# Optimization experiments

Measured on AMD Instinct MI355X. Metric: run time of the kernel, lower is better.

The kernel has to match this reference:

```python
import jax, jax.numpy as jnp
import numpy as np

B, N, D, H = 4, 8192, 1024, 16
C = D // H  # head dim = 64
EPS = 1e-6


def setup_inputs() -> dict:
    key = jax.random.key(0)
    ks = jax.random.split(key, 8)
    sc = 0.02
    return {
        "q": jax.random.normal(ks[0], (B, N, D), jnp.float32),
        "k": jax.random.normal(ks[1], (B, N, D), jnp.float32),
        "v": jax.random.normal(ks[2], (B, N, D), jnp.float32),
        "Wq": jax.random.normal(ks[3], (D, D), jnp.float32) * sc,
        "Wk": jax.random.normal(ks[4], (D, D), jnp.float32) * sc,
        "Wv": jax.random.normal(ks[5], (D, D), jnp.float32) * sc,
        "Wproj": jax.random.normal(ks[6], (D, D), jnp.float32) * sc,
        "focusing_factor": jnp.asarray(3.0, jnp.float32),
    }


def _to_heads(x):
    # b n (h c) -> (b h) n c
    return x.reshape(B, N, H, C).transpose(0, 2, 1, 3).reshape(B * H, N, C)


def reference(q, k, v, Wq, Wk, Wv, Wproj, focusing_factor):
    # projections (torch Linear: x @ W.T, no bias)
    qp = q @ Wq.T
    kp = k @ Wk.T
    vp = v @ Wv.T

    def feature_map(x):
        # |GELU(x)| + eps, then focused renormalization:
        # softmax(focusing_factor * log(f)) * mean(f)
        f = jnp.abs(jax.nn.gelu(x, approximate=False)) + EPS
        f_norm = f.mean(axis=-1, keepdims=True)
        return jax.nn.softmax(jnp.log(f) * focusing_factor, axis=-1) * f_norm

    qf = feature_map(qp)
    kf = feature_map(kp)

    qh = _to_heads(qf)  # [B*H, N, C]
    kh = _to_heads(kf)
    vh = _to_heads(vp)

    k_mean = kh.mean(axis=1)  # [B*H, C]
    z_inv = jnp.einsum('bnd,bd->bn', qh, k_mean) + EPS  # [B*H, N]

    # (k/sqrt(N))^T (v/sqrt(N)) == (k^T v)/N
    kv = jnp.einsum('bnc,bnd->bcd', kh, vh) / N  # [B*H, C, C]
    y = jnp.einsum('bic,bcd->bid', qh, kv) / z_inv[..., None]  # [B*H, N, C]

    y = y.reshape(B, H, N, C).transpose(0, 2, 1, 3).reshape(B, N, D)
    return y @ Wproj.T
```

## Files before the change

kernel.cpp:

```cpp
#include <hip/hip_runtime.h>

using f16 = _Float16;
typedef __attribute__((ext_vector_type(4))) _Float16 f16x4;
typedef __attribute__((ext_vector_type(8))) _Float16 f16x8;
typedef __attribute__((ext_vector_type(4))) float f32x4;

#define DEVI __device__ __forceinline__

namespace {

constexpr int BB = 4;
constexpr int NN = 8192;
constexpr int DD = 1024;
constexpr int MTOT = BB * NN;
constexpr float FSCALE = 64.0f;
constexpr float ZCONST = 64.0f * 64.0f * (8192.0f * 1e-6f);

DEVI void gl16(const void* g, void* l) {
  __builtin_amdgcn_global_load_lds(
      (__attribute__((address_space(1))) void*)(void*)g,
      (__attribute__((address_space(3))) void*)l, 16, 0, 0);
}

DEVI float wsum(float v) {
#pragma unroll
  for (int m = 32; m > 0; m >>= 1) v += __shfl_xor(v, m, 64);
  return v;
}
DEVI float wmaxr(float v) {
#pragma unroll
  for (int m = 32; m > 0; m >>= 1) v = fmaxf(v, __shfl_xor(v, m, 64));
  return v;
}
DEVI float block_sum(float v, float* sred, int tid) {
  v = wsum(v);
  __syncthreads();
  if ((tid & 63) == 0) sred[tid >> 6] = v;
  __syncthreads();
  return sred[0] + sred[1] + sred[2] + sred[3];
}
DEVI float block_max(float v, float* sred, int tid) {
  v = wmaxr(v);
  __syncthreads();
  if ((tid & 63) == 0) sred[tid >> 6] = v;
  __syncthreads();
  return fmaxf(fmaxf(sred[0], sred[1]), fmaxf(sred[2], sred[3]));
}

struct CastArgs {
  const float* src[8];
  f16* dst[8];
  int n4[8];
};

__global__ __launch_bounds__(256) void cast_kernel(CastArgs a) {
  const int z = blockIdx.y;
  const float4* __restrict__ s = (const float4*)a.src[z];
  f16x4* __restrict__ d = (f16x4*)a.dst[z];
  const int n4 = a.n4[z];
  for (int i = blockIdx.x * blockDim.x + threadIdx.x; i < n4;
       i += gridDim.x * blockDim.x) {
    float4 f = s[i];
    f16x4 o = {(f16)f.x, (f16)f.y, (f16)f.z, (f16)f.w};
    d[i] = o;
  }
}

struct Gemm3 {
  const f16* A[3];
  const f16* Bt[3];
  void* C[3];
};

template <typename OutT>
__global__ __launch_bounds__(512, 2) void gemm256(Gemm3 P) {
  constexpr int K = DD;
  constexpr int N = DD;
  constexpr int NKT = K / 64;
  const int z = blockIdx.z;
  const f16* __restrict__ A = P.A[z];
  const f16* __restrict__ Bt = P.Bt[z];
  OutT* __restrict__ C = (OutT*)P.C[z];

  const int nx = gridDim.x;
  int lin = blockIdx.y * nx + blockIdx.x;
  const int cpx = (gridDim.y * nx) >> 3;
  lin = (lin & 7) * cpx + (lin >> 3);
  const size_t row0 = (size_t)(lin / nx) * 256;
  const size_t col0 = (size_t)(lin % nx) * 256;

  const int tid = threadIdx.x, lane = tid & 63, wv = tid >> 6;
  const int wm = wv >> 2, wn = wv & 3;
  const int fr = lane & 15, f7 = lane & 7, kq = lane >> 4;

  __shared__ __align__(16) f16 LA[2][2][8192];
  __shared__ __align__(16) f16 LB[2][2][8192];

  const int srow = wv * 8 + (lane >> 3);
  const int ssw = (lane & 7) ^ ((lane >> 3) & 7);

  auto stageA = [&](int kts, int half) {
    const f16* src = A + (row0 + half * 128 + srow) * K + kts * 64 + ssw * 8;
    f16* dst = &LA[kts & 1][half][wv * 512];
#pragma unroll
    for (int c = 0; c < 2; ++c) gl16(src + (size_t)c * 64 * K, dst + c * 4096);
  };
  auto stageB = [&](int kts, int half) {
    const f16* src = Bt + (col0 + half * 128 + srow) * K + kts * 64 + ssw * 8;
    f16* dst = &LB[kts & 1][half][wv * 512];
#pragma unroll
    for (int c = 0; c < 2; ++c) gl16(src + (size_t)c * 64 * K, dst + c * 4096);
  };

  f32x4 acc[8][4];
#pragma unroll
  for (int i = 0; i < 8; ++i)
#pragma unroll
    for (int j = 0; j < 4; ++j) acc[i][j] = f32x4{0.f, 0.f, 0.f, 0.f};

  stageA(0, 0); stageA(0, 1); stageB(0, 0); stageB(0, 1);
  stageA(1, 0); stageA(1, 1);
  asm volatile("s_waitcnt vmcnt(4)" ::: "memory");
  __builtin_amdgcn_s_barrier();

  const int c0e = (kq ^ f7) * 8;
#pragma unroll 2
  for (int kt = 0; kt < NKT; ++kt) {
    const int buf = kt & 1;
    const f16* Ah = LA[buf][wm];
    const f16* Bh = &LB[buf][wn >> 1][(wn & 1) * 4096];
    f16x8 a0[8], a1[8], b0[4], b1[4];

#pragma unroll
    for (int mi = 0; mi < 8; ++mi)
      a0[mi] = *(const f16x8*)&Ah[(mi * 16 + fr) * 64 + c0e];
#pragma unroll
    for (int ni = 0; ni < 4; ++ni)
      b0[ni] = *(const f16x8*)&Bh[(ni * 16 + fr) * 64 + c0e];
    if (kt < NKT - 1) stageB(kt + 1, 0);
    __builtin_amdgcn_s_barrier();
    asm volatile("s_waitcnt lgkmcnt(0)" ::: "memory");
    __builtin_amdgcn_s_setprio(1);
#pragma unroll
    for (int mi = 0; mi < 4; ++mi)
#pragma unroll
      for (int ni = 0; ni < 4; ++ni)
        acc[mi][ni] = __builtin_amdgcn_mfma_f32_16x16x32_f16(
            a0[mi], b0[ni], acc[mi][ni], 0, 0, 0);
    __builtin_amdgcn_s_setprio(0);
    __builtin_amdgcn_s_barrier();

#pragma unroll
    for (int mi = 0; mi < 8; ++mi)
      a1[mi] = *(const f16x8*)&Ah[(mi * 16 + fr) * 64 + (c0e ^ 32)];
    if (kt < NKT - 1) stageB(kt + 1, 1);
    __builtin_amdgcn_s_barrier();
    asm volatile("s_waitcnt lgkmcnt(0)" ::: "memory");
    __builtin_amdgcn_s_setprio(1);
#pragma unroll
    for (int mi = 4; mi < 8; ++mi)
#pragma unroll
      for (int ni = 0; ni < 4; ++ni)
        acc[mi][ni] = __builtin_amdgcn_mfma_f32_16x16x32_f16(
            a0[mi], b0[ni], acc[mi][ni], 0, 0, 0);
    __builtin_amdgcn_s_setprio(0);
    __builtin_amdgcn_s_barrier();

#pragma unroll
    for (int ni = 0; ni < 4; ++ni)
      b1[ni] = *(const f16x8*)&Bh[(ni * 16 + fr) * 64 + (c0e ^ 32)];
    if (kt < NKT - 2) stageA(kt + 2, 0);
    __builtin_amdgcn_s_barrier();
    asm volatile("s_waitcnt lgkmcnt(0)" ::: "memory");
    __builtin_amdgcn_s_setprio(1);
#pragma unroll
    for (int mi = 0; mi < 4; ++mi)
#pragma unroll
      for (int ni = 0; ni < 4; ++ni)
        acc[mi][ni] = __builtin_amdgcn_mfma_f32_16x16x32_f16(
            a1[mi], b1[ni], acc[mi][ni], 0, 0, 0);
    __builtin_amdgcn_s_setprio(0);
    __builtin_amdgcn_s_barrier();

    if (kt < NKT - 2) stageA(kt + 2, 1);
    __builtin_amdgcn_s_barrier();
    __builtin_amdgcn_s_setprio(1);
#pragma unroll
    for (int mi = 4; mi < 8; ++mi)
#pragma unroll
      for (int ni = 0; ni < 4; ++ni)
        acc[mi][ni] = __builtin_amdgcn_mfma_f32_16x16x32_f16(
            a1[mi], b1[ni], acc[mi][ni], 0, 0, 0);
    __builtin_amdgcn_s_setprio(0);
    if (kt < NKT - 2)
      asm volatile("s_waitcnt vmcnt(4)" ::: "memory");
    else
      asm volatile("s_waitcnt vmcnt(0)" ::: "memory");
    __builtin_amdgcn_s_barrier();
  }

#pragma unroll
  for (int mi = 0; mi < 8; ++mi)
#pragma unroll
    for (int ni = 0; ni < 4; ++ni) {
      const size_t colv = col0 + wn * 64 + ni * 16 + fr;
#pragma unroll
      for (int r = 0; r < 4; ++r) {
        const size_t rowv = row0 + wm * 128 + mi * 16 + (lane >> 4) * 4 + r;
        C[rowv * N + colv] = (OutT)acc[mi][ni][r];
      }
    }
}

__global__ __launch_bounds__(256) void feature_kernel(
    const f16* __restrict__ qp, const f16* __restrict__ kp,
    f16* __restrict__ qf, f16* __restrict__ kf, const float* __restrict__ ffp) {
  const int row = blockIdx.x;
  const int tid = threadIdx.x;
  const bool isq = (blockIdx.y == 0);
  const f16* __restrict__ src = isq ? qp : kp;
  f16* __restrict__ dst = isq ? qf : kf;
  const float ff = ffp[0];
  __shared__ float sred[4];

  f16x4 xv = ((const f16x4*)src)[(size_t)row * 256 + tid];
  float f0[4];
  float ps = 0.f;
#pragma unroll
  for (int j = 0; j < 4; ++j) {
    float x = (float)xv[j];
    float g = 0.5f * x * (1.0f + erff(x * 0.70710678118654752f));
    float fv = fabsf(g) + 1e-6f;
    f0[j] = fv;
    ps += fv;
  }
  float fsum = block_sum(ps, sred, tid);
  float t[4];
  float pm = -1e30f;
#pragma unroll
  for (int j = 0; j < 4; ++j) {
    t[j] = ff * __logf(f0[j]);
    pm = fmaxf(pm, t[j]);
  }
  float tmax = block_max(pm, sred, tid);
  float e[4];
  float es = 0.f;
#pragma unroll
  for (int j = 0; j < 4; ++j) {
    e[j] = __expf(t[j] - tmax);
    es += e[j];
  }
  float esum = block_sum(es, sred, tid);
  const float scale = fsum * (1.0f / 1024.0f) / esum * FSCALE;
  f16x4 o;
#pragma unroll
  for (int j = 0; j < 4; ++j) o[j] = (f16)(e[j] * scale);
  ((f16x4*)dst)[(size_t)row * 256 + tid] = o;
}

__global__ __launch_bounds__(256) void kv_kernel(
    const f16* __restrict__ kf, const f16* __restrict__ vp,
    float* __restrict__ kvsum, float* __restrict__ colsum) {
  const int bh = blockIdx.x;
  const int b = bh >> 4, h = bh & 15;
  const int tid = threadIdx.x, lane = tid & 63, wave = tid >> 6;
  __shared__ __align__(16) f16 kt[32 * 64];
  __shared__ __align__(16) f16 vt[32 * 64];
  __shared__ float csred[4][64];

  f32x4 acc[4];
#pragma unroll
  for (int ni = 0; ni < 4; ++ni) acc[ni] = f32x4{0.f, 0.f, 0.f, 0.f};
  float cpart = 0.f;

  const int srow = wave * 8 + (lane >> 3);
  const int scol = (lane & 7) * 8;
  const int colbase = h * 64;
  const int n0base = blockIdx.y * 512;

  for (int n0 = n0base; n0 < n0base + 512; n0 += 32) {
    const size_t gofs = ((size_t)(b * NN + n0 + srow)) * DD + colbase + scol;
    gl16(kf + gofs, &kt[wave * 512]);
    gl16(vp + gofs, &vt[wave * 512]);
    __syncthreads();
    {
      const int c = tid & 63;
      const int r0 = (tid >> 6) * 8;
#pragma unroll
      for (int rr = 0; rr < 8; ++rr) cpart += (float)kt[(r0 + rr) * 64 + c];
    }
    f16x8 a, bfr[4];
#pragma unroll
    for (int j = 0; j < 8; ++j)
      a[j] = kt[((lane >> 4) * 8 + j) * 64 + wave * 16 + (lane & 15)];
#pragma unroll
    for (int ni = 0; ni < 4; ++ni)
#pragma unroll
      for (int j = 0; j < 8; ++j)
        bfr[ni][j] = vt[((lane >> 4) * 8 + j) * 64 + ni * 16 + (lane & 15)];
#pragma unroll
    for (int ni = 0; ni < 4; ++ni)
      acc[ni] = __builtin_amdgcn_mfma_f32_16x16x32_f16(a, bfr[ni], acc[ni], 0, 0, 0);
    __syncthreads();
  }
#pragma unroll
  for (int ni = 0; ni < 4; ++ni)
#pragma unroll
    for (int r = 0; r < 4; ++r) {
      const int c = wave * 16 + (lane >> 4) * 4 + r;
      const int d = ni * 16 + (lane & 15);
      atomicAdd(&kvsum[(size_t)bh * 4096 + c * 64 + d], acc[ni][r]);
    }
  csred[tid >> 6][tid & 63] = cpart;
  __syncthreads();
  if (tid < 64)
    atomicAdd(&colsum[bh * 64 + tid],
              csred[0][tid] + csred[1][tid] + csred[2][tid] + csred[3][tid]);
}

__global__ __launch_bounds__(256) void y_kernel(
    const f16* __restrict__ qf, const f16* __restrict__ kv16,
    const float* __restrict__ colsum, f16* __restrict__ y) {
  const int bh = blockIdx.x, b = bh >> 4, h = bh & 15;
  const int n0 = blockIdx.y * 128;
  const int tid = threadIdx.x, lane = tid & 63, wave = tid >> 6;
  __shared__ __align__(16) f16 qs[128 * 64];
  __shared__ __align__(16) f16 kvs[64 * 64];
  __shared__ float cs[64];
  __shared__ float zr[128];

#pragma unroll
  for (int cc = 0; cc < 4; ++cc) {
    const int r = wave * 32 + cc * 8 + (lane >> 3);
    gl16(qf + ((size_t)(b * NN + n0 + r)) * DD + h * 64 + (lane & 7) * 8,
         &qs[(wave * 4 + cc) * 512]);
  }
#pragma unroll
  for (int cc = 0; cc < 2; ++cc) {
    const int r = wave * 16 + cc * 8 + (lane >> 3);
    gl16(kv16 + (size_t)bh * 4096 + r * 64 + (lane & 7) * 8,
         &kvs[(wave * 2 + cc) * 512]);
  }
  if (tid < 64) cs[tid] = colsum[bh * 64 + tid];
  __syncthreads();
  if (tid < 128) {
    float zv = 0.f;
    for (int cc = 0; cc < 64; ++cc) {
      const int c = (cc + tid) & 63;
      zv += (float)qs[tid * 64 + c] * cs[c];
    }
    zr[tid] = zv + ZCONST;
  }
  __syncthreads();

  f32x4 acc[2][4];
#pragma unroll
  for (int mi = 0; mi < 2; ++mi)
#pragma unroll
    for (int ni = 0; ni < 4; ++ni) acc[mi][ni] = f32x4{0.f, 0.f, 0.f, 0.f};

#pragma unroll
  for (int ks = 0; ks < 2; ++ks) {
    f16x8 a[2], bfr[4];
#pragma unroll
    for (int mi = 0; mi < 2; ++mi)
      a[mi] = *(const f16x8*)&qs[(wave * 32 + mi * 16 + (lane & 15)) * 64 +
                                 ks * 32 + (lane >> 4) * 8];
#pragma unroll
    for (int ni = 0; ni < 4; ++ni)
#pragma unroll
      for (int j = 0; j < 8; ++j)
        bfr[ni][j] = kvs[(ks * 32 + (lane >> 4) * 8 + j) * 64 + ni * 16 + (lane & 15)];
#pragma unroll
    for (int mi = 0; mi < 2; ++mi)
#pragma unroll
      for (int ni = 0; ni < 4; ++ni)
        acc[mi][ni] = __builtin_amdgcn_mfma_f32_16x16x32_f16(
            a[mi], bfr[ni], acc[mi][ni], 0, 0, 0);
  }
#pragma unroll
  for (int mi = 0; mi < 2; ++mi)
#pragma unroll
    for (int ni = 0; ni < 4; ++ni)
#pragma unroll
      for (int r = 0; r < 4; ++r) {
        const int rrow = wave * 32 + mi * 16 + (lane >> 4) * 4 + r;
        const int d = ni * 16 + (lane & 15);
        const float yv = acc[mi][ni][r] / zr[rrow];
        y[((size_t)(b * NN + n0 + rrow)) * DD + h * 64 + d] = (f16)yv;
      }
}

}

extern "C" void kernel_launch(void* const* d_in, const int* in_sizes, int n_in,
                              void* d_out, int out_size, void* d_ws, size_t ws_size,
                              hipStream_t stream) {
  const float* q = (const float*)d_in[0];
  const float* k = (const float*)d_in[1];
  const float* v = (const float*)d_in[2];
  const float* Wq = (const float*)d_in[3];
  const float* Wk = (const float*)d_in[4];
  const float* Wv = (const float*)d_in[5];
  const float* Wp = (const float*)d_in[6];
  const float* ffp = (const float*)d_in[7];

  char* w = (char*)d_ws;
  size_t off = 0;
  auto alloc = [&](size_t b) {
    void* p = (void*)(w + off);
    off += (b + 255) & ~(size_t)255;
    return p;
  };
  const size_t big = (size_t)MTOT * DD * sizeof(f16);
  f16* q16 = (f16*)alloc(big);
  f16* k16 = (f16*)alloc(big);
  f16* v16 = (f16*)alloc(big);
  f16* qp16 = (f16*)alloc(big);
  f16* kp16 = (f16*)alloc(big);
  f16* vp16 = (f16*)alloc(big);
  f16* Wq16 = (f16*)alloc((size_t)DD * DD * 2);
  f16* Wk16 = (f16*)alloc((size_t)DD * DD * 2);
  f16* Wv16 = (f16*)alloc((size_t)DD * DD * 2);
  f16* Wp16 = (f16*)alloc((size_t)DD * DD * 2);
  float* kvsum = (float*)alloc(64 * 64 * 64 * sizeof(float));
  float* colsum = (float*)alloc(64 * 64 * sizeof(float));
  f16* kv16 = (f16*)alloc(64 * 64 * 64 * sizeof(f16));
  if (off > ws_size) return;

  f16* qf = q16;
  f16* kf = k16;
  f16* y16 = v16;

  CastArgs ca{};
  ca.src[0] = q;  ca.dst[0] = q16;  ca.n4[0] = MTOT * DD / 4;
  ca.src[1] = k;  ca.dst[1] = k16;  ca.n4[1] = MTOT * DD / 4;
  ca.src[2] = v;  ca.dst[2] = v16;  ca.n4[2] = MTOT * DD / 4;
  ca.src[3] = Wq; ca.dst[3] = Wq16; ca.n4[3] = DD * DD / 4;
  ca.src[4] = Wk; ca.dst[4] = Wk16; ca.n4[4] = DD * DD / 4;
  ca.src[5] = Wv; ca.dst[5] = Wv16; ca.n4[5] = DD * DD / 4;
  ca.src[6] = Wp; ca.dst[6] = Wp16; ca.n4[6] = DD * DD / 4;
  cast_kernel<<<dim3(1024, 7), 256, 0, stream>>>(ca);

  Gemm3 gp{};
  gp.A[0] = q16; gp.Bt[0] = Wq16; gp.C[0] = qp16;
  gp.A[1] = k16; gp.Bt[1] = Wk16; gp.C[1] = kp16;
  gp.A[2] = v16; gp.Bt[2] = Wv16; gp.C[2] = vp16;
  gemm256<f16><<<dim3(DD / 256, MTOT / 256, 3), 512, 0, stream>>>(gp);

  feature_kernel<<<dim3(MTOT, 2), 256, 0, stream>>>(qp16, kp16, qf, kf, ffp);

  hipMemsetAsync(kvsum, 0, 64 * 64 * 64 * sizeof(float) + 64 * 64 * sizeof(float),
                 stream);
  kv_kernel<<<dim3(64, 16), 256, 0, stream>>>(kf, vp16, kvsum, colsum);

  CastArgs cb{};
  cb.src[0] = kvsum; cb.dst[0] = kv16; cb.n4[0] = 64 * 64 * 64 / 4;
  cast_kernel<<<dim3(64, 1), 256, 0, stream>>>(cb);

  y_kernel<<<dim3(64, 64), 256, 0, stream>>>(qf, kv16, colsum, y16);

  Gemm3 gf{};
  gf.A[0] = y16; gf.Bt[0] = Wp16; gf.C[0] = d_out;
  gemm256<float><<<dim3(DD / 256, MTOT / 256, 1), 512, 0, stream>>>(gf);
}
```

Baseline: 700.3 us.

## Restructure GEMM main loop to single-barrier one-ahead prefetch

The GEMM inner loop now issues the whole next k-tile (A and B halves) into the alternate LDS buffer at the start of each iteration. It then loads all A/B fragments for both k-halves up front and runs the MFMAs in two batches gated by partial lgkmcnt waits, with a single barrier per iteration. This replaces the previous schedule, which used four interleaved barriers and prefetched A two tiles ahead. The aim is to cut barrier and synchronisation overhead and let the MFMAs issue in longer runs. The cost is a shallower prefetch distance for A and higher register pressure from holding all fragments at once.

```diff
diff --git a/kernel.cpp b/kernel.cpp
--- a/kernel.cpp
+++ b/kernel.cpp
@@ -119,83 +119,59 @@
     for (int j = 0; j < 4; ++j) acc[i][j] = f32x4{0.f, 0.f, 0.f, 0.f};
 
   stageA(0, 0); stageA(0, 1); stageB(0, 0); stageB(0, 1);
-  stageA(1, 0); stageA(1, 1);
-  asm volatile("s_waitcnt vmcnt(4)" ::: "memory");
+  asm volatile("s_waitcnt vmcnt(0)" ::: "memory");
   __builtin_amdgcn_s_barrier();
 
   const int c0e = (kq ^ f7) * 8;
+
 #pragma unroll 2
   for (int kt = 0; kt < NKT; ++kt) {
     const int buf = kt & 1;
     const f16* Ah = LA[buf][wm];
     const f16* Bh = &LB[buf][wn >> 1][(wn & 1) * 4096];
+
+    if (kt + 1 < NKT) {
+      stageA(kt + 1, 0); stageA(kt + 1, 1);
+      stageB(kt + 1, 0); stageB(kt + 1, 1);
+    }
+
     f16x8 a0[8], a1[8], b0[4], b1[4];
-
 #pragma unroll
     for (int mi = 0; mi < 8; ++mi)
       a0[mi] = *(const f16x8*)&Ah[(mi * 16 + fr) * 64 + c0e];
 #pragma unroll
     for (int ni = 0; ni < 4; ++ni)
       b0[ni] = *(const f16x8*)&Bh[(ni * 16 + fr) * 64 + c0e];
-    if (kt < NKT - 1) stageB(kt + 1, 0);
-    __builtin_amdgcn_s_barrier();
-    asm volatile("s_waitcnt lgkmcnt(0)" ::: "memory");
+#pragma unroll
+    for (int mi = 0; mi < 8; ++mi)
+      a1[mi] = *(const f16x8*)&Ah[(mi * 16 + fr) * 64 + (c0e ^ 32)];
+#pragma unroll
+    for (int ni = 0; ni < 4; ++ni)
+      b1[ni] = *(const f16x8*)&Bh[(ni * 16 + fr) * 64 + (c0e ^ 32)];
+
+    asm volatile("s_waitcnt lgkmcnt(12)" ::: "memory");
+    __builtin_amdgcn_sched_barrier(0);
     __builtin_amdgcn_s_setprio(1);
 #pragma unroll
-    for (int mi = 0; mi < 4; ++mi)
+    for (int mi = 0; mi < 8; ++mi)
 #pragma unroll
       for (int ni = 0; ni < 4; ++ni)
         acc[mi][ni] = __builtin_amdgcn_mfma_f32_16x16x32_f16(
             a0[mi], b0[ni], acc[mi][ni], 0, 0, 0);
     __builtin_amdgcn_s_setprio(0);
-    __builtin_amdgcn_s_barrier();
-
+
+    asm volatile("s_waitcnt lgkmcnt(0)" ::: "memory");
+    __builtin_amdgcn_sched_barrier(0);
+    __builtin_amdgcn_s_setprio(1);
 #pragma unroll
     for (int mi = 0; mi < 8; ++mi)
-      a1[mi] = *(const f16x8*)&Ah[(mi * 16 + fr) * 64 + (c0e ^ 32)];
-    if (kt < NKT - 1) stageB(kt + 1, 1);
-    __builtin_amdgcn_s_barrier();
-    asm volatile("s_waitcnt lgkmcnt(0)" ::: "memory");
-    __builtin_amdgcn_s_setprio(1);
-#pragma unroll
-    for (int mi = 4; mi < 8; ++mi)
-#pragma unroll
-      for (int ni = 0; ni < 4; ++ni)
-        acc[mi][ni] = __builtin_amdgcn_mfma_f32_16x16x32_f16(
-            a0[mi], b0[ni], acc[mi][ni], 0, 0, 0);
-    __builtin_amdgcn_s_setprio(0);
-    __builtin_amdgcn_s_barrier();
-
-#pragma unroll
-    for (int ni = 0; ni < 4; ++ni)
-      b1[ni] = *(const f16x8*)&Bh[(ni * 16 + fr) * 64 + (c0e ^ 32)];
-    if (kt < NKT - 2) stageA(kt + 2, 0);
-    __builtin_amdgcn_s_barrier();
-    asm volatile("s_waitcnt lgkmcnt(0)" ::: "memory");
-    __builtin_amdgcn_s_setprio(1);
-#pragma unroll
-    for (int mi = 0; mi < 4; ++mi)
 #pragma unroll
       for (int ni = 0; ni < 4; ++ni)
         acc[mi][ni] = __builtin_amdgcn_mfma_f32_16x16x32_f16(
             a1[mi], b1[ni], acc[mi][ni], 0, 0, 0);
     __builtin_amdgcn_s_setprio(0);
-    __builtin_amdgcn_s_barrier();
-
-    if (kt < NKT - 2) stageA(kt + 2, 1);
-    __builtin_amdgcn_s_barrier();
-    __builtin_amdgcn_s_setprio(1);
-#pragma unroll
-    for (int mi = 4; mi < 8; ++mi)
-#pragma unroll
-      for (int ni = 0; ni < 4; ++ni)
-        acc[mi][ni] = __builtin_amdgcn_mfma_f32_16x16x32_f16(
-            a1[mi], b1[ni], acc[mi][ni], 0, 0, 0);
-    __builtin_amdgcn_s_setprio(0);
-    if (kt < NKT - 2)
-      asm volatile("s_waitcnt vmcnt(4)" ::: "memory");
-    else
-      asm volatile("s_waitcnt vmcnt(0)" ::: "memory");
+
+    asm volatile("s_waitcnt vmcnt(0)" ::: "memory");
     __builtin_amdgcn_s_barrier();
   }
 
```

After: 693.3 us. About the same (-1.0%).

## Fuse fp32-to-fp16 activation cast into QKV projection GEMM A-loads

Applied to the files above, without the earlier changes.

The projection GEMM now reads fp32 activations straight from global memory into registers, converts them to fp16 and writes them into swizzled LDS, so the separate cast pass over q, k and v is no longer needed. Only the weights are still cast by the standalone cast kernel. This removes a full write and re-read of three 64MB fp16 copies. In exchange, A loads go through registers instead of direct-to-LDS loads, which raises VGPR pressure and adds a synchronous wait and LDS write each k-step. Sched barriers are also added to both GEMM variants, and the unroll-2 pragma on the original GEMM loop is dropped.

```diff
diff --git a/kernel.cpp b/kernel.cpp
--- a/kernel.cpp
+++ b/kernel.cpp
@@ -71,33 +71,181 @@
   const f16* Bt[3];
   void* C[3];
 };
+struct Gemm3f {
+  const float* A[3];
+  const f16* Bt[3];
+  f16* C[3];
+};
+
+#define GEMM_PREAMBLE()                                                      \
+  constexpr int K = DD;                                                      \
+  constexpr int N = DD;                                                      \
+  constexpr int NKT = K / 64;                                                \
+  const int nx = gridDim.x;                                                  \
+  int lin = blockIdx.y * nx + blockIdx.x;                                    \
+  const int cpx = (gridDim.y * nx) >> 3;                                     \
+  lin = (lin & 7) * cpx + (lin >> 3);                                        \
+  const size_t row0 = (size_t)(lin / nx) * 256;                              \
+  const size_t col0 = (size_t)(lin % nx) * 256;                              \
+  const int tid = threadIdx.x, lane = tid & 63, wv = tid >> 6;               \
+  const int wm = wv >> 2, wn = wv & 3;                                       \
+  const int fr = lane & 15, f7 = lane & 7, kq = lane >> 4;                   \
+  const int srow = wv * 8 + (lane >> 3);                                     \
+  const int ssw = (lane & 7) ^ ((lane >> 3) & 7);                            \
+  const int c0e = (kq ^ f7) * 8;
+
+__global__ __launch_bounds__(512, 2) void gemm256_fa(Gemm3f P) {
+  GEMM_PREAMBLE()
+  const int z = blockIdx.z;
+  const float* __restrict__ A = P.A[z];
+  const f16* __restrict__ Bt = P.Bt[z];
+  f16* __restrict__ C = P.C[z];
+
+  __shared__ __align__(16) f16 LA[2][2][8192];
+  __shared__ __align__(16) f16 LB[2][2][8192];
+
+  auto stageB = [&](int kts, int half) {
+    const f16* src = Bt + (col0 + half * 128 + srow) * K + kts * 64 + ssw * 8;
+    f16* dst = &LB[kts & 1][half][wv * 512];
+#pragma unroll
+    for (int c = 0; c < 2; ++c) gl16(src + (size_t)c * 64 * K, dst + c * 4096);
+  };
+
+  const int ar = tid >> 2;
+  const int ac2 = (tid & 3) * 2;
+  auto loadA = [&](int kts, int half, float4* r) {
+    const float* src = A + (row0 + half * 128 + ar) * (size_t)K + kts * 64;
+#pragma unroll
+    for (int c = 0; c < 2; ++c) {
+      r[2 * c + 0] = *(const float4*)(src + (ac2 + c) * 8);
+      r[2 * c + 1] = *(const float4*)(src + (ac2 + c) * 8 + 4);
+    }
+  };
+  auto writeA = [&](int kts, int half, const float4* r) {
+    f16* base = &LA[kts & 1][half][ar * 64];
+#pragma unroll
+    for (int c = 0; c < 2; ++c) {
+      const float4 lo = r[2 * c], hi = r[2 * c + 1];
+      f16x8 o = {(f16)lo.x, (f16)lo.y, (f16)lo.z, (f16)lo.w,
+                 (f16)hi.x, (f16)hi.y, (f16)hi.z, (f16)hi.w};
+      *(f16x8*)&base[((ac2 + c) ^ (ar & 7)) * 8] = o;
+    }
+  };
+
+  f32x4 acc[8][4];
+#pragma unroll
+  for (int i = 0; i < 8; ++i)
+#pragma unroll
+    for (int j = 0; j < 4; ++j) acc[i][j] = f32x4{0.f, 0.f, 0.f, 0.f};
+
+  float4 ra0[4], ra1[4];
+  loadA(0, 0, ra0); loadA(0, 1, ra1);
+  stageB(0, 0); stageB(0, 1);
+  asm volatile("s_waitcnt vmcnt(0)" ::: "memory");
+  writeA(0, 0, ra0); writeA(0, 1, ra1);
+  asm volatile("s_waitcnt lgkmcnt(0)" ::: "memory");
+  __builtin_amdgcn_s_barrier();
+
+  for (int kt = 0; kt < NKT; ++kt) {
+    const int buf = kt & 1;
+    const f16* Ah = LA[buf][wm];
+    const f16* Bh = &LB[buf][wn >> 1][(wn & 1) * 4096];
+    f16x8 a0[8], a1[8], b0[4], b1[4];
+
+#pragma unroll
+    for (int mi = 0; mi < 8; ++mi)
+      a0[mi] = *(const f16x8*)&Ah[(mi * 16 + fr) * 64 + c0e];
+#pragma unroll
+    for (int ni = 0; ni < 4; ++ni)
+      b0[ni] = *(const f16x8*)&Bh[(ni * 16 + fr) * 64 + c0e];
+    if (kt + 1 < NKT) stageB(kt + 1, 0);
+    __builtin_amdgcn_s_barrier();
+    asm volatile("s_waitcnt lgkmcnt(0)" ::: "memory");
+    __builtin_amdgcn_sched_barrier(0);
+    __builtin_amdgcn_s_setprio(1);
+#pragma unroll
+    for (int mi = 0; mi < 4; ++mi)
+#pragma unroll
+      for (int ni = 0; ni < 4; ++ni)
+        acc[mi][ni] = __builtin_amdgcn_mfma_f32_16x16x32_f16(
+            a0[mi], b0[ni], acc[mi][ni], 0, 0, 0);
+    __builtin_amdgcn_s_setprio(0);
+    __builtin_amdgcn_s_barrier();
+
+#pragma unroll
+    for (int mi = 0; mi < 8; ++mi)
+      a1[mi] = *(const f16x8*)&Ah[(mi * 16 + fr) * 64 + (c0e ^ 32)];
+    if (kt + 1 < NKT) stageB(kt + 1, 1);
+    __builtin_amdgcn_s_barrier();
+    asm volatile("s_waitcnt lgkmcnt(0)" ::: "memory");
+    __builtin_amdgcn_sched_barrier(0);
+    __builtin_amdgcn_s_setprio(1);
+#pragma unroll
+    for (int mi = 4; mi < 8; ++mi)
+#pragma unroll
+      for (int ni = 0; ni < 4; ++ni)
+        acc[mi][ni] = __builtin_amdgcn_mfma_f32_16x16x32_f16(
+            a0[mi], b0[ni], acc[mi][ni], 0, 0, 0);
+    __builtin_amdgcn_s_setprio(0);
+    __builtin_amdgcn_s_barrier();
+
+#pragma unroll
+    for (int ni = 0; ni < 4; ++ni)
+      b1[ni] = *(const f16x8*)&Bh[(ni * 16 + fr) * 64 + (c0e ^ 32)];
+    if (kt + 1 < NKT) { loadA(kt + 1, 0, ra0); loadA(kt + 1, 1, ra1); }
+    __builtin_amdgcn_s_barrier();
+    asm volatile("s_waitcnt lgkmcnt(0)" ::: "memory");
+    __builtin_amdgcn_sched_barrier(0);
+    __builtin_amdgcn_s_setprio(1);
+#pragma unroll
+    for (int mi = 0; mi < 4; ++mi)
+#pragma unroll
+      for (int ni = 0; ni < 4; ++ni)
+        acc[mi][ni] = __builtin_amdgcn_mfma_f32_16x16x32_f16(
+            a1[mi], b1[ni], acc[mi][ni], 0, 0, 0);
+    __builtin_amdgcn_s_setprio(0);
+    __builtin_amdgcn_s_barrier();
+
+    __builtin_amdgcn_s_setprio(1);
+#pragma unroll
+    for (int mi = 4; mi < 8; ++mi)
+#pragma unroll
+      for (int ni = 0; ni < 4; ++ni)
+        acc[mi][ni] = __builtin_amdgcn_mfma_f32_16x16x32_f16(
+            a1[mi], b1[ni], acc[mi][ni], 0, 0, 0);
+    __builtin_amdgcn_s_setprio(0);
+    if (kt + 1 < NKT) {
+      asm volatile("s_waitcnt vmcnt(0)" ::: "memory");
+      __builtin_amdgcn_sched_barrier(0);
+      writeA(kt + 1, 0, ra0); writeA(kt + 1, 1, ra1);
+      asm volatile("s_waitcnt lgkmcnt(0)" ::: "memory");
+    }
+    __builtin_amdgcn_s_barrier();
+  }
+
+#pragma unroll
+  for (int mi = 0; mi < 8; ++mi)
+#pragma unroll
+    for (int ni = 0; ni < 4; ++ni) {
+      const size_t colv = col0 + wn * 64 + ni * 16 + fr;
+#pragma unroll
+      for (int r = 0; r < 4; ++r) {
+        const size_t rowv = row0 + wm * 128 + mi * 16 + (lane >> 4) * 4 + r;
+        C[rowv * N + colv] = (f16)acc[mi][ni][r];
+      }
+    }
+}
 
 template <typename OutT>
 __global__ __launch_bounds__(512, 2) void gemm256(Gemm3 P) {
-  constexpr int K = DD;
-  constexpr int N = DD;
-  constexpr int NKT = K / 64;
+  GEMM_PREAMBLE()
   const int z = blockIdx.z;
   const f16* __restrict__ A = P.A[z];
   const f16* __restrict__ Bt = P.Bt[z];
   OutT* __restrict__ C = (OutT*)P.C[z];
 
-  const int nx = gridDim.x;
-  int lin = blockIdx.y * nx + blockIdx.x;
-  const int cpx = (gridDim.y * nx) >> 3;
-  lin = (lin & 7) * cpx + (lin >> 3);
-  const size_t row0 = (size_t)(lin / nx) * 256;
-  const size_t col0 = (size_t)(lin % nx) * 256;
-
-  const int tid = threadIdx.x, lane = tid & 63, wv = tid >> 6;
-  const int wm = wv >> 2, wn = wv & 3;
-  const int fr = lane & 15, f7 = lane & 7, kq = lane >> 4;
-
   __shared__ __align__(16) f16 LA[2][2][8192];
   __shared__ __align__(16) f16 LB[2][2][8192];
-
-  const int srow = wv * 8 + (lane >> 3);
-  const int ssw = (lane & 7) ^ ((lane >> 3) & 7);
 
   auto stageA = [&](int kts, int half) {
     const f16* src = A + (row0 + half * 128 + srow) * K + kts * 64 + ssw * 8;
@@ -123,8 +271,6 @@
   asm volatile("s_waitcnt vmcnt(4)" ::: "memory");
   __builtin_amdgcn_s_barrier();
 
-  const int c0e = (kq ^ f7) * 8;
-#pragma unroll 2
   for (int kt = 0; kt < NKT; ++kt) {
     const int buf = kt & 1;
     const f16* Ah = LA[buf][wm];
@@ -140,6 +286,7 @@
     if (kt < NKT - 1) stageB(kt + 1, 0);
     __builtin_amdgcn_s_barrier();
     asm volatile("s_waitcnt lgkmcnt(0)" ::: "memory");
+    __builtin_amdgcn_sched_barrier(0);
     __builtin_amdgcn_s_setprio(1);
 #pragma unroll
     for (int mi = 0; mi < 4; ++mi)
@@ -156,6 +303,7 @@
     if (kt < NKT - 1) stageB(kt + 1, 1);
     __builtin_amdgcn_s_barrier();
     asm volatile("s_waitcnt lgkmcnt(0)" ::: "memory");
+    __builtin_amdgcn_sched_barrier(0);
     __builtin_amdgcn_s_setprio(1);
 #pragma unroll
     for (int mi = 4; mi < 8; ++mi)
@@ -172,6 +320,7 @@
     if (kt < NKT - 2) stageA(kt + 2, 0);
     __builtin_amdgcn_s_barrier();
     asm volatile("s_waitcnt lgkmcnt(0)" ::: "memory");
+    __builtin_amdgcn_sched_barrier(0);
     __builtin_amdgcn_s_setprio(1);
 #pragma unroll
     for (int mi = 0; mi < 4; ++mi)
@@ -413,12 +562,12 @@
     return p;
   };
   const size_t big = (size_t)MTOT * DD * sizeof(f16);
-  f16* q16 = (f16*)alloc(big);
-  f16* k16 = (f16*)alloc(big);
-  f16* v16 = (f16*)alloc(big);
   f16* qp16 = (f16*)alloc(big);
   f16* kp16 = (f16*)alloc(big);
   f16* vp16 = (f16*)alloc(big);
+  f16* qf  = (f16*)alloc(big);
+  f16* kf  = (f16*)alloc(big);
+  f16* y16 = (f16*)alloc(big);
   f16* Wq16 = (f16*)alloc((size_t)DD * DD * 2);
   f16* Wk16 = (f16*)alloc((size_t)DD * DD * 2);
   f16* Wv16 = (f16*)alloc((size_t)DD * DD * 2);
@@ -428,25 +577,18 @@
   f16* kv16 = (f16*)alloc(64 * 64 * 64 * sizeof(f16));
   if (off > ws_size) return;
 
-  f16* qf = q16;
-  f16* kf = k16;
-  f16* y16 = v16;
-
   CastArgs ca{};
-  ca.src[0] = q;  ca.dst[0] = q16;  ca.n4[0] = MTOT * DD / 4;
-  ca.src[1] = k;  ca.dst[1] = k16;  ca.n4[1] = MTOT * DD / 4;
-  ca.src[2] = v;  ca.dst[2] = v16;  ca.n4[2] = MTOT * DD / 4;
-  ca.src[3] = Wq; ca.dst[3] = Wq16; ca.n4[3] = DD * DD / 4;
-  ca.src[4] = Wk; ca.dst[4] = Wk16; ca.n4[4] = DD * DD / 4;
-  ca.src[5] = Wv; ca.dst[5] = Wv16; ca.n4[5] = DD * DD / 4;
-  ca.src[6] = Wp; ca.dst[6] = Wp16; ca.n4[6] = DD * DD / 4;
-  cast_kernel<<<dim3(1024, 7), 256, 0, stream>>>(ca);
-
-  Gemm3 gp{};
-  gp.A[0] = q16; gp.Bt[0] = Wq16; gp.C[0] = qp16;
-  gp.A[1] = k16; gp.Bt[1] = Wk16; gp.C[1] = kp16;
-  gp.A[2] = v16; gp.Bt[2] = Wv16; gp.C[2] = vp16;
-  gemm256<f16><<<dim3(DD / 256, MTOT / 256, 3), 512, 0, stream>>>(gp);
+  ca.src[0] = Wq; ca.dst[0] = Wq16; ca.n4[0] = DD * DD / 4;
+  ca.src[1] = Wk; ca.dst[1] = Wk16; ca.n4[1] = DD * DD / 4;
+  ca.src[2] = Wv; ca.dst[2] = Wv16; ca.n4[2] = DD * DD / 4;
+  ca.src[3] = Wp; ca.dst[3] = Wp16; ca.n4[3] = DD * DD / 4;
+  cast_kernel<<<dim3(128, 4), 256, 0, stream>>>(ca);
+
+  Gemm3f gp{};
+  gp.A[0] = q; gp.Bt[0] = Wq16; gp.C[0] = qp16;
+  gp.A[1] = k; gp.Bt[1] = Wk16; gp.C[1] = kp16;
+  gp.A[2] = v; gp.Bt[2] = Wv16; gp.C[2] = vp16;
+  gemm256_fa<<<dim3(DD / 256, MTOT / 256, 3), 512, 0, stream>>>(gp);
 
   feature_kernel<<<dim3(MTOT, 2), 256, 0, stream>>>(qp16, kp16, qf, kf, ffp);
 
```

Result: faster. 663.1 us (-5.3%).
